# Kernel optimization log

Hardware: AMD Instinct MI355X
Metric: run time of the kernel (lower is better)

The kernel has to match this reference:

```python
import jax, jax.numpy as jnp
import numpy as np

A = 100000   # batched action space size
V = 500000   # relation vocab
D = 128      # ExperimentSettings.dim
L = 64       # question token count


def setup_inputs() -> dict:
    key = jax.random.key(0)
    ks = jax.random.split(key, 8)
    return {
        "action_ids": jax.random.randint(ks[0], (A,), 0, V),
        "emb_table": jax.random.normal(ks[1], (V, D), dtype=jnp.float32) * 0.1,
        "question_t": jax.random.normal(ks[2], (L, D), dtype=jnp.float32),
        "history_t": jax.random.normal(ks[3], (D,), dtype=jnp.float32),
        "W1": jax.random.normal(ks[4], (D, 2 * D), dtype=jnp.float32) * 0.05,
        "b1": jnp.zeros((D,), dtype=jnp.float32),
        "W2": jax.random.normal(ks[5], (D, D), dtype=jnp.float32) * 0.05,
        "b2": jnp.zeros((D,), dtype=jnp.float32),
    }


def reference(action_ids, emb_table, question_t, history_t, W1, b1, W2, b2):
    # per-action relation embedding lookup (batched over the action space)
    rel = emb_table[action_ids]                              # [A, D]
    # attention over question tokens, keyed by the relation embedding
    att = jnp.einsum("ld,ad->al", question_t, rel)           # [A, L]
    w = jax.nn.softmax(att, axis=-1)
    question = jnp.einsum("al,ld->ad", w, question_t)        # [A, D]
    # Perceptron(dim, dim, 2*dim): MLP on [history; question], dotted with rel
    hist = jnp.broadcast_to(history_t, question.shape)       # [A, D]
    x = jnp.concatenate([hist, question], axis=-1)           # [A, 2D]
    hidden = jax.nn.relu(x @ W1.T + b1)                      # [A, D]
    out = hidden @ W2.T + b2                                 # [A, D]
    scores = jnp.sum(rel * out, axis=-1)                     # [A]
    return jax.nn.softmax(scores, axis=0)
```

## Files before the change

kernel.cpp:

```cpp
#include <hip/hip_runtime.h>
#include <math.h>


#define BA   64
#define NTHR 256

typedef float          f32x4  __attribute__((ext_vector_type(4)));
typedef short          bf16x8 __attribute__((ext_vector_type(8)));
typedef unsigned short us4v   __attribute__((ext_vector_type(4)));

#define RELo 0
#define R1o  8704
#define R2o  17408
#define R3o  26624
#define NB   31232

__device__ __forceinline__ unsigned short f2bf(float f) {
    unsigned int u = __float_as_uint(f);
    return (unsigned short)((u + 0x7fffu + ((u >> 16) & 1u)) >> 16);
}
__device__ __forceinline__ float bf2f(unsigned short h) {
    return __uint_as_float(((unsigned int)h) << 16);
}

__global__ void k_prep(const float* __restrict__ hist, const float* __restrict__ W1,
                       const float* __restrict__ b1, float* __restrict__ h1)
{
    const int lane = threadIdx.x & 63;
    const int w    = threadIdx.x >> 6;
    const float h0  = hist[lane];
    const float h64 = hist[64 + lane];
    #pragma unroll 4
    for (int r = 0; r < 32; ++r) {
        const int j = w * 32 + r;
        float p = fmaf(W1[j * 256 + lane], h0, W1[j * 256 + 64 + lane] * h64);
        #pragma unroll
        for (int o = 1; o < 64; o <<= 1) p += __shfl_xor(p, o);
        if (lane == 0) h1[j] = b1[j] + p;
    }
}

__global__ void __launch_bounds__(NTHR, 2)
k_main(const int* __restrict__ action_ids,
       const float* __restrict__ emb,
       const float* __restrict__ Qg,
       const float* __restrict__ W1,
       const float* __restrict__ W2,
       const float* __restrict__ b2,
       const float* __restrict__ h1g,
       float* __restrict__ scores,
       float* __restrict__ mb,
       float* __restrict__ sb,
       int A)
{
    __shared__ __align__(16) unsigned short B_[NB];
    __shared__ float h1s[128];
    __shared__ float b2s[128];
    __shared__ float stash[BA];

    const int tid  = threadIdx.x;
    const int a0   = blockIdx.x * BA;
    const int w    = tid >> 6;
    const int lane = tid & 63;
    const int c    = lane & 15;
    const int g    = lane >> 4;

    {
        const int l = tid >> 2, seg = tid & 3;
        const float4* qs = (const float4*)&Qg[l * 128 + seg * 32];
        unsigned short qb[32];
        #pragma unroll
        for (int j = 0; j < 8; ++j) {
            const float4 v = qs[j];
            qb[j*4+0] = f2bf(v.x); qb[j*4+1] = f2bf(v.y);
            qb[j*4+2] = f2bf(v.z); qb[j*4+3] = f2bf(v.w);
            us4v p = { qb[j*4+0], qb[j*4+1], qb[j*4+2], qb[j*4+3] };
            *(us4v*)&B_[R1o + l * 136 + seg * 32 + j * 4] = p;
        }
        #pragma unroll
        for (int i = 0; i < 32; ++i)
            B_[R2o + (seg * 32 + i) * 72 + l] = qb[i];

        const int ga  = a0 + l;
        const int rid = (ga < A) ? action_ids[ga] : 0;
        const float4* es = (const float4*)&emb[(size_t)rid * 128 + seg * 32];
        #pragma unroll
        for (int j = 0; j < 8; ++j) {
            const float4 v = es[j];
            us4v p = { f2bf(v.x), f2bf(v.y), f2bf(v.z), f2bf(v.w) };
            *(us4v*)&B_[RELo + l * 136 + seg * 32 + j * 4] = p;
        }
        if (tid < 128) h1s[tid] = h1g[tid];
        else           b2s[tid - 128] = b2[tid - 128];
    }
    __syncthreads();

    f32x4 att[4] = {};
    #pragma unroll
    for (int ks = 0; ks < 4; ++ks) {
        const bf16x8 afr = *(const bf16x8*)&B_[RELo + (16*w + c)*136 + ks*32 + g*8];
        #pragma unroll
        for (int nt = 0; nt < 4; ++nt) {
            const bf16x8 bfr = *(const bf16x8*)&B_[R1o + (16*nt + c)*136 + ks*32 + g*8];
            att[nt] = __builtin_amdgcn_mfma_f32_16x16x32_bf16(afr, bfr, att[nt], 0, 0, 0);
        }
    }

    {
        float m[4] = { -INFINITY, -INFINITY, -INFINITY, -INFINITY };
        #pragma unroll
        for (int nt = 0; nt < 4; ++nt)
            #pragma unroll
            for (int r = 0; r < 4; ++r) m[r] = fmaxf(m[r], att[nt][r]);
        #pragma unroll
        for (int r = 0; r < 4; ++r) {
            m[r] = fmaxf(m[r], __shfl_xor(m[r], 1));
            m[r] = fmaxf(m[r], __shfl_xor(m[r], 2));
            m[r] = fmaxf(m[r], __shfl_xor(m[r], 4));
            m[r] = fmaxf(m[r], __shfl_xor(m[r], 8));
        }
        float s[4] = { 0.f, 0.f, 0.f, 0.f };
        #pragma unroll
        for (int nt = 0; nt < 4; ++nt)
            #pragma unroll
            for (int r = 0; r < 4; ++r) {
                att[nt][r] = __expf(att[nt][r] - m[r]);
                s[r] += att[nt][r];
            }
        #pragma unroll
        for (int r = 0; r < 4; ++r) {
            s[r] += __shfl_xor(s[r], 1);
            s[r] += __shfl_xor(s[r], 2);
            s[r] += __shfl_xor(s[r], 4);
            s[r] += __shfl_xor(s[r], 8);
            s[r] = 1.f / s[r];
        }
        #pragma unroll
        for (int nt = 0; nt < 4; ++nt)
            #pragma unroll
            for (int r = 0; r < 4; ++r)
                B_[R3o + (16*w + 4*g + r)*72 + 16*nt + c] =
                    f2bf(att[nt][r] * s[r]);
    }

    f32x4 qacc[8] = {};
    #pragma unroll
    for (int ks = 0; ks < 2; ++ks) {
        const bf16x8 afr = *(const bf16x8*)&B_[R3o + (16*w + c)*72 + ks*32 + g*8];
        #pragma unroll
        for (int nt = 0; nt < 8; ++nt) {
            const bf16x8 bfr = *(const bf16x8*)&B_[R2o + (16*nt + c)*72 + ks*32 + g*8];
            qacc[nt] = __builtin_amdgcn_mfma_f32_16x16x32_bf16(afr, bfr, qacc[nt], 0, 0, 0);
        }
    }
    __syncthreads();

    #pragma unroll
    for (int nt = 0; nt < 8; ++nt)
        #pragma unroll
        for (int r = 0; r < 4; ++r)
            B_[R1o + (16*w + 4*g + r)*136 + 16*nt + c] = f2bf(qacc[nt][r]);

    f32x4 hacc[8] = {};
    for (int ch = 0; ch < 4; ++ch) {
        if (ch) __syncthreads();
        {
            const int jl = tid >> 3, seg = tid & 7;
            const float4* src = (const float4*)&W1[(ch*32 + jl)*256 + 128 + seg*16];
            #pragma unroll
            for (int j = 0; j < 4; ++j) {
                const float4 v = src[j];
                us4v p = { f2bf(v.x), f2bf(v.y), f2bf(v.z), f2bf(v.w) };
                *(us4v*)&B_[R3o + jl*136 + seg*16 + j*4] = p;
            }
        }
        __syncthreads();
        #pragma unroll
        for (int ks = 0; ks < 4; ++ks) {
            const bf16x8 afr = *(const bf16x8*)&B_[R1o + (16*w + c)*136 + ks*32 + g*8];
            #pragma unroll
            for (int nt = 0; nt < 2; ++nt) {
                const bf16x8 bfr = *(const bf16x8*)&B_[R3o + (16*nt + c)*136 + ks*32 + g*8];
                hacc[ch*2+nt] = __builtin_amdgcn_mfma_f32_16x16x32_bf16(afr, bfr, hacc[ch*2+nt], 0, 0, 0);
            }
        }
    }
    __syncthreads();

    #pragma unroll
    for (int ch = 0; ch < 4; ++ch)
        #pragma unroll
        for (int nt = 0; nt < 2; ++nt) {
            const int j = ch*32 + nt*16 + c;
            const float hb = h1s[j];
            #pragma unroll
            for (int r = 0; r < 4; ++r) {
                const float hv = fmaxf(hacc[ch*2+nt][r] + hb, 0.f);
                B_[R2o + (16*w + 4*g + r)*136 + j] = f2bf(hv);
            }
        }

    float sacc[4] = { 0.f, 0.f, 0.f, 0.f };
    for (int ch = 0; ch < 4; ++ch) {
        if (ch) __syncthreads();
        {
            const int dl = tid >> 3, seg = tid & 7;
            const float4* src = (const float4*)&W2[(ch*32 + dl)*128 + seg*16];
            #pragma unroll
            for (int j = 0; j < 4; ++j) {
                const float4 v = src[j];
                us4v p = { f2bf(v.x), f2bf(v.y), f2bf(v.z), f2bf(v.w) };
                *(us4v*)&B_[R3o + dl*136 + seg*16 + j*4] = p;
            }
        }
        __syncthreads();
        f32x4 oacc[2] = {};
        #pragma unroll
        for (int ks = 0; ks < 4; ++ks) {
            const bf16x8 afr = *(const bf16x8*)&B_[R2o + (16*w + c)*136 + ks*32 + g*8];
            #pragma unroll
            for (int nt = 0; nt < 2; ++nt) {
                const bf16x8 bfr = *(const bf16x8*)&B_[R3o + (16*nt + c)*136 + ks*32 + g*8];
                oacc[nt] = __builtin_amdgcn_mfma_f32_16x16x32_bf16(afr, bfr, oacc[nt], 0, 0, 0);
            }
        }
        #pragma unroll
        for (int nt = 0; nt < 2; ++nt) {
            const int d = ch*32 + nt*16 + c;
            const float bb = b2s[d];
            #pragma unroll
            for (int r = 0; r < 4; ++r) {
                const float ov = oacc[nt][r] + bb;
                const float rv = bf2f(B_[RELo + (16*w + 4*g + r)*136 + d]);
                sacc[r] = fmaf(ov, rv, sacc[r]);
            }
        }
    }

    #pragma unroll
    for (int r = 0; r < 4; ++r) {
        sacc[r] += __shfl_xor(sacc[r], 1);
        sacc[r] += __shfl_xor(sacc[r], 2);
        sacc[r] += __shfl_xor(sacc[r], 4);
        sacc[r] += __shfl_xor(sacc[r], 8);
    }
    if (c == 0) {
        #pragma unroll
        for (int r = 0; r < 4; ++r) {
            const int al = 16*w + 4*g + r;
            const int ga = a0 + al;
            if (ga < A) scores[ga] = sacc[r];
            stash[al] = sacc[r];
        }
    }
    __syncthreads();

    if (tid < 64) {
        const bool valid = (a0 + tid) < A;
        float sv = valid ? stash[tid] : -INFINITY;
        float m = sv;
        #pragma unroll
        for (int o = 1; o < 64; o <<= 1) m = fmaxf(m, __shfl_xor(m, o));
        float ex = valid ? __expf(sv - m) : 0.f;
        #pragma unroll
        for (int o = 1; o < 64; o <<= 1) ex += __shfl_xor(ex, o);
        if (tid == 0) { mb[blockIdx.x] = m; sb[blockIdx.x] = ex; }
    }
}

__global__ void k_combine(const float* __restrict__ mb, const float* __restrict__ sb,
                          int n, float* __restrict__ MS)
{
    __shared__ float red[256];
    const int tid = threadIdx.x;
    float m = -INFINITY;
    for (int i = tid; i < n; i += 256) m = fmaxf(m, mb[i]);
    red[tid] = m; __syncthreads();
    for (int s = 128; s > 0; s >>= 1) {
        if (tid < s) red[tid] = fmaxf(red[tid], red[tid + s]);
        __syncthreads();
    }
    const float M = red[0];
    __syncthreads();
    float sum = 0.f;
    for (int i = tid; i < n; i += 256) sum += sb[i] * __expf(mb[i] - M);
    red[tid] = sum; __syncthreads();
    for (int s = 128; s > 0; s >>= 1) {
        if (tid < s) red[tid] += red[tid + s];
        __syncthreads();
    }
    if (tid == 0) { MS[0] = M; MS[1] = 1.f / red[0]; }
}

__global__ void k_norm(const float* __restrict__ scores, const float* __restrict__ MS,
                       float* __restrict__ out, int A)
{
    const int i = blockIdx.x * blockDim.x + threadIdx.x;
    if (i < A) out[i] = __expf(scores[i] - MS[0]) * MS[1];
}

extern "C" void kernel_launch(void* const* d_in, const int* in_sizes, int n_in,
                              void* d_out, int out_size, void* d_ws, size_t ws_size,
                              hipStream_t stream)
{
    const int*   action_ids = (const int*)  d_in[0];
    const float* emb        = (const float*)d_in[1];
    const float* Qg         = (const float*)d_in[2];
    const float* hist       = (const float*)d_in[3];
    const float* W1         = (const float*)d_in[4];
    const float* b1         = (const float*)d_in[5];
    const float* W2         = (const float*)d_in[6];
    const float* b2         = (const float*)d_in[7];
    float* out = (float*)d_out;
    const int A    = in_sizes[0];
    const int nblk = (A + BA - 1) / BA;

    float* ws  = (float*)d_ws;
    float* h1  = ws;
    float* MS  = ws + 128;
    const int nal = (nblk + 255) & ~255;
    float* mbp = ws + 256;
    float* sbp = mbp + nal;
    (void)n_in; (void)out_size; (void)ws_size;

    k_prep<<<1, 256, 0, stream>>>(hist, W1, b1, h1);
    k_main<<<nblk, NTHR, 0, stream>>>(action_ids, emb, Qg, W1, W2, b2, h1,
                                      out, mbp, sbp, A);
    k_combine<<<1, 256, 0, stream>>>(mbp, sbp, nblk, MS);
    k_norm<<<(A + 255) / 256, 256, 0, stream>>>(out, MS, out, A);
}
```

Measured before the change: 388.9 us.

## Preconvert weights to bf16 once and make each wave independent without block syncs

A new pre-kernel converts Q, Q transpose, and the W1/W2 halves to bf16 in workspace once per call. The main kernel then reads MFMA B-fragments directly from global/L2 instead of staging and converting weights in LDS every block. Each wave now owns its own 16-row LDS slice, which removes all __syncthreads. LDS use drops enough to raise the launch-bounds occupancy to 4, and softmax partials are emitted per wave. The cost is an extra launch and more scattered global fragment loads that depend on L2 caching.

```diff
diff --git a/kernel.cpp b/kernel.cpp
--- a/kernel.cpp
+++ b/kernel.cpp
@@ -4,22 +4,18 @@
 
 #define BA   64
 #define NTHR 256
-
-typedef float          f32x4  __attribute__((ext_vector_type(4)));
-typedef short          bf16x8 __attribute__((ext_vector_type(8)));
-typedef unsigned short us4v   __attribute__((ext_vector_type(4)));
-
-#define RELo 0
-#define R1o  8704
-#define R2o  17408
-#define R3o  26624
-#define NB   31232
-
-__device__ __forceinline__ unsigned short f2bf(float f) {
+typedef unsigned short ushort_t;
+typedef float  f32x4  __attribute__((ext_vector_type(4)));
+typedef short  bf16x8 __attribute__((ext_vector_type(8)));
+
+#define WSTRIDE 4352
+#define LDS_USH (4 * WSTRIDE)
+
+__device__ __forceinline__ ushort_t f2bf(float f) {
     unsigned int u = __float_as_uint(f);
-    return (unsigned short)((u + 0x7fffu + ((u >> 16) & 1u)) >> 16);
-}
-__device__ __forceinline__ float bf2f(unsigned short h) {
+    return (ushort_t)((u + 0x7fffu + ((u >> 16) & 1u)) >> 16);
+}
+__device__ __forceinline__ float bf2f(ushort_t h) {
     return __uint_as_float(((unsigned int)h) << 16);
 }
 
@@ -40,71 +36,78 @@
     }
 }
 
-__global__ void __launch_bounds__(NTHR, 2)
+__global__ void k_cvt(const float* __restrict__ Qg, const float* __restrict__ W1,
+                      const float* __restrict__ W2,
+                      ushort_t* __restrict__ Qbf, ushort_t* __restrict__ QTbf,
+                      ushort_t* __restrict__ W1bf, ushort_t* __restrict__ W2bf)
+{
+    const int i = blockIdx.x * 256 + threadIdx.x;
+    if (i < 16384) {
+        W1bf[i] = f2bf(W1[(i >> 7) * 256 + 128 + (i & 127)]);
+    } else if (i < 32768) {
+        const int k = i - 16384;
+        W2bf[k] = f2bf(W2[k]);
+    } else if (i < 40960) {
+        const int k = i - 32768;
+        Qbf[k] = f2bf(Qg[k]);
+    } else {
+        const int k = i - 40960;
+        const int d = k >> 6, l = k & 63;
+        QTbf[k] = f2bf(Qg[l * 128 + d]);
+    }
+}
+
+__global__ void __launch_bounds__(NTHR, 4)
 k_main(const int* __restrict__ action_ids,
        const float* __restrict__ emb,
-       const float* __restrict__ Qg,
-       const float* __restrict__ W1,
-       const float* __restrict__ W2,
        const float* __restrict__ b2,
        const float* __restrict__ h1g,
+       const ushort_t* __restrict__ Qbf,
+       const ushort_t* __restrict__ QTbf,
+       const ushort_t* __restrict__ W1bf,
+       const ushort_t* __restrict__ W2bf,
        float* __restrict__ scores,
        float* __restrict__ mb,
        float* __restrict__ sb,
        int A)
 {
-    __shared__ __align__(16) unsigned short B_[NB];
-    __shared__ float h1s[128];
-    __shared__ float b2s[128];
-    __shared__ float stash[BA];
-
+    __shared__ __align__(16) ushort_t L[LDS_USH];
     const int tid  = threadIdx.x;
-    const int a0   = blockIdx.x * BA;
     const int w    = tid >> 6;
     const int lane = tid & 63;
     const int c    = lane & 15;
     const int g    = lane >> 4;
-
+    ushort_t* RELw = &L[w * WSTRIDE];
+    ushort_t* SCRw = &L[w * WSTRIDE + 2176];
+    const int a0   = blockIdx.x * BA + 16 * w;
+
+    bf16x8 relA[4];
     {
-        const int l = tid >> 2, seg = tid & 3;
-        const float4* qs = (const float4*)&Qg[l * 128 + seg * 32];
-        unsigned short qb[32];
-        #pragma unroll
-        for (int j = 0; j < 8; ++j) {
-            const float4 v = qs[j];
-            qb[j*4+0] = f2bf(v.x); qb[j*4+1] = f2bf(v.y);
-            qb[j*4+2] = f2bf(v.z); qb[j*4+3] = f2bf(v.w);
-            us4v p = { qb[j*4+0], qb[j*4+1], qb[j*4+2], qb[j*4+3] };
-            *(us4v*)&B_[R1o + l * 136 + seg * 32 + j * 4] = p;
-        }
-        #pragma unroll
-        for (int i = 0; i < 32; ++i)
-            B_[R2o + (seg * 32 + i) * 72 + l] = qb[i];
-
-        const int ga  = a0 + l;
+        const int ga  = a0 + c;
         const int rid = (ga < A) ? action_ids[ga] : 0;
-        const float4* es = (const float4*)&emb[(size_t)rid * 128 + seg * 32];
-        #pragma unroll
-        for (int j = 0; j < 8; ++j) {
-            const float4 v = es[j];
-            us4v p = { f2bf(v.x), f2bf(v.y), f2bf(v.z), f2bf(v.w) };
-            *(us4v*)&B_[RELo + l * 136 + seg * 32 + j * 4] = p;
-        }
-        if (tid < 128) h1s[tid] = h1g[tid];
-        else           b2s[tid - 128] = b2[tid - 128];
-    }
-    __syncthreads();
+        const float* er = emb + (size_t)rid * 128;
+        #pragma unroll
+        for (int ks = 0; ks < 4; ++ks) {
+            const float4 v0 = *(const float4*)&er[ks * 32 + g * 8];
+            const float4 v1 = *(const float4*)&er[ks * 32 + g * 8 + 4];
+            union { bf16x8 v; ushort_t u[8]; } p;
+            p.u[0] = f2bf(v0.x); p.u[1] = f2bf(v0.y);
+            p.u[2] = f2bf(v0.z); p.u[3] = f2bf(v0.w);
+            p.u[4] = f2bf(v1.x); p.u[5] = f2bf(v1.y);
+            p.u[6] = f2bf(v1.z); p.u[7] = f2bf(v1.w);
+            relA[ks] = p.v;
+            *(bf16x8*)&RELw[c * 136 + ks * 32 + g * 8] = p.v;
+        }
+    }
 
     f32x4 att[4] = {};
     #pragma unroll
-    for (int ks = 0; ks < 4; ++ks) {
-        const bf16x8 afr = *(const bf16x8*)&B_[RELo + (16*w + c)*136 + ks*32 + g*8];
+    for (int ks = 0; ks < 4; ++ks)
         #pragma unroll
         for (int nt = 0; nt < 4; ++nt) {
-            const bf16x8 bfr = *(const bf16x8*)&B_[R1o + (16*nt + c)*136 + ks*32 + g*8];
-            att[nt] = __builtin_amdgcn_mfma_f32_16x16x32_bf16(afr, bfr, att[nt], 0, 0, 0);
-        }
-    }
+            const bf16x8 bfr = *(const bf16x8*)&Qbf[(16*nt + c) * 128 + ks*32 + g*8];
+            att[nt] = __builtin_amdgcn_mfma_f32_16x16x32_bf16(relA[ks], bfr, att[nt], 0, 0, 0);
+        }
 
     {
         float m[4] = { -INFINITY, -INFINITY, -INFINITY, -INFINITY };
@@ -139,104 +142,64 @@
         for (int nt = 0; nt < 4; ++nt)
             #pragma unroll
             for (int r = 0; r < 4; ++r)
-                B_[R3o + (16*w + 4*g + r)*72 + 16*nt + c] =
-                    f2bf(att[nt][r] * s[r]);
+                SCRw[(4*g + r) * 72 + 16*nt + c] = f2bf(att[nt][r] * s[r]);
     }
 
     f32x4 qacc[8] = {};
     #pragma unroll
     for (int ks = 0; ks < 2; ++ks) {
-        const bf16x8 afr = *(const bf16x8*)&B_[R3o + (16*w + c)*72 + ks*32 + g*8];
+        const bf16x8 afr = *(const bf16x8*)&SCRw[c * 72 + ks*32 + g*8];
         #pragma unroll
         for (int nt = 0; nt < 8; ++nt) {
-            const bf16x8 bfr = *(const bf16x8*)&B_[R2o + (16*nt + c)*72 + ks*32 + g*8];
+            const bf16x8 bfr = *(const bf16x8*)&QTbf[(16*nt + c) * 64 + ks*32 + g*8];
             qacc[nt] = __builtin_amdgcn_mfma_f32_16x16x32_bf16(afr, bfr, qacc[nt], 0, 0, 0);
         }
     }
-    __syncthreads();
-
     #pragma unroll
     for (int nt = 0; nt < 8; ++nt)
         #pragma unroll
         for (int r = 0; r < 4; ++r)
-            B_[R1o + (16*w + 4*g + r)*136 + 16*nt + c] = f2bf(qacc[nt][r]);
+            SCRw[(4*g + r) * 136 + 16*nt + c] = f2bf(qacc[nt][r]);
 
     f32x4 hacc[8] = {};
-    for (int ch = 0; ch < 4; ++ch) {
-        if (ch) __syncthreads();
-        {
-            const int jl = tid >> 3, seg = tid & 7;
-            const float4* src = (const float4*)&W1[(ch*32 + jl)*256 + 128 + seg*16];
-            #pragma unroll
-            for (int j = 0; j < 4; ++j) {
-                const float4 v = src[j];
-                us4v p = { f2bf(v.x), f2bf(v.y), f2bf(v.z), f2bf(v.w) };
-                *(us4v*)&B_[R3o + jl*136 + seg*16 + j*4] = p;
-            }
-        }
-        __syncthreads();
-        #pragma unroll
-        for (int ks = 0; ks < 4; ++ks) {
-            const bf16x8 afr = *(const bf16x8*)&B_[R1o + (16*w + c)*136 + ks*32 + g*8];
-            #pragma unroll
-            for (int nt = 0; nt < 2; ++nt) {
-                const bf16x8 bfr = *(const bf16x8*)&B_[R3o + (16*nt + c)*136 + ks*32 + g*8];
-                hacc[ch*2+nt] = __builtin_amdgcn_mfma_f32_16x16x32_bf16(afr, bfr, hacc[ch*2+nt], 0, 0, 0);
-            }
-        }
-    }
-    __syncthreads();
-
-    #pragma unroll
-    for (int ch = 0; ch < 4; ++ch)
-        #pragma unroll
-        for (int nt = 0; nt < 2; ++nt) {
-            const int j = ch*32 + nt*16 + c;
-            const float hb = h1s[j];
-            #pragma unroll
-            for (int r = 0; r < 4; ++r) {
-                const float hv = fmaxf(hacc[ch*2+nt][r] + hb, 0.f);
-                B_[R2o + (16*w + 4*g + r)*136 + j] = f2bf(hv);
-            }
-        }
-
+    #pragma unroll
+    for (int ks = 0; ks < 4; ++ks) {
+        const bf16x8 afr = *(const bf16x8*)&SCRw[c * 136 + ks*32 + g*8];
+        #pragma unroll
+        for (int nt = 0; nt < 8; ++nt) {
+            const bf16x8 bfr = *(const bf16x8*)&W1bf[(16*nt + c) * 128 + ks*32 + g*8];
+            hacc[nt] = __builtin_amdgcn_mfma_f32_16x16x32_bf16(afr, bfr, hacc[nt], 0, 0, 0);
+        }
+    }
+    #pragma unroll
+    for (int nt = 0; nt < 8; ++nt) {
+        const float hb = h1g[16*nt + c];
+        #pragma unroll
+        for (int r = 0; r < 4; ++r)
+            SCRw[(4*g + r) * 136 + 16*nt + c] = f2bf(fmaxf(hacc[nt][r] + hb, 0.f));
+    }
+
+    f32x4 oacc[8] = {};
+    #pragma unroll
+    for (int ks = 0; ks < 4; ++ks) {
+        const bf16x8 afr = *(const bf16x8*)&SCRw[c * 136 + ks*32 + g*8];
+        #pragma unroll
+        for (int nt = 0; nt < 8; ++nt) {
+            const bf16x8 bfr = *(const bf16x8*)&W2bf[(16*nt + c) * 128 + ks*32 + g*8];
+            oacc[nt] = __builtin_amdgcn_mfma_f32_16x16x32_bf16(afr, bfr, oacc[nt], 0, 0, 0);
+        }
+    }
     float sacc[4] = { 0.f, 0.f, 0.f, 0.f };
-    for (int ch = 0; ch < 4; ++ch) {
-        if (ch) __syncthreads();
-        {
-            const int dl = tid >> 3, seg = tid & 7;
-            const float4* src = (const float4*)&W2[(ch*32 + dl)*128 + seg*16];
-            #pragma unroll
-            for (int j = 0; j < 4; ++j) {
-                const float4 v = src[j];
-                us4v p = { f2bf(v.x), f2bf(v.y), f2bf(v.z), f2bf(v.w) };
-                *(us4v*)&B_[R3o + dl*136 + seg*16 + j*4] = p;
-            }
-        }
-        __syncthreads();
-        f32x4 oacc[2] = {};
-        #pragma unroll
-        for (int ks = 0; ks < 4; ++ks) {
-            const bf16x8 afr = *(const bf16x8*)&B_[R2o + (16*w + c)*136 + ks*32 + g*8];
-            #pragma unroll
-            for (int nt = 0; nt < 2; ++nt) {
-                const bf16x8 bfr = *(const bf16x8*)&B_[R3o + (16*nt + c)*136 + ks*32 + g*8];
-                oacc[nt] = __builtin_amdgcn_mfma_f32_16x16x32_bf16(afr, bfr, oacc[nt], 0, 0, 0);
-            }
-        }
-        #pragma unroll
-        for (int nt = 0; nt < 2; ++nt) {
-            const int d = ch*32 + nt*16 + c;
-            const float bb = b2s[d];
-            #pragma unroll
-            for (int r = 0; r < 4; ++r) {
-                const float ov = oacc[nt][r] + bb;
-                const float rv = bf2f(B_[RELo + (16*w + 4*g + r)*136 + d]);
-                sacc[r] = fmaf(ov, rv, sacc[r]);
-            }
-        }
-    }
-
+    #pragma unroll
+    for (int nt = 0; nt < 8; ++nt) {
+        const float bb = b2[16*nt + c];
+        #pragma unroll
+        for (int r = 0; r < 4; ++r) {
+            const float ov = oacc[nt][r] + bb;
+            const float rv = bf2f(RELw[(4*g + r) * 136 + 16*nt + c]);
+            sacc[r] = fmaf(ov, rv, sacc[r]);
+        }
+    }
     #pragma unroll
     for (int r = 0; r < 4; ++r) {
         sacc[r] += __shfl_xor(sacc[r], 1);
@@ -247,24 +210,29 @@
     if (c == 0) {
         #pragma unroll
         for (int r = 0; r < 4; ++r) {
-            const int al = 16*w + 4*g + r;
-            const int ga = a0 + al;
+            const int ga = a0 + 4*g + r;
             if (ga < A) scores[ga] = sacc[r];
-            stash[al] = sacc[r];
-        }
-    }
-    __syncthreads();
-
-    if (tid < 64) {
-        const bool valid = (a0 + tid) < A;
-        float sv = valid ? stash[tid] : -INFINITY;
-        float m = sv;
-        #pragma unroll
-        for (int o = 1; o < 64; o <<= 1) m = fmaxf(m, __shfl_xor(m, o));
-        float ex = valid ? __expf(sv - m) : 0.f;
-        #pragma unroll
-        for (int o = 1; o < 64; o <<= 1) ex += __shfl_xor(ex, o);
-        if (tid == 0) { mb[blockIdx.x] = m; sb[blockIdx.x] = ex; }
+        }
+    }
+
+    {
+        float m = -INFINITY;
+        #pragma unroll
+        for (int r = 0; r < 4; ++r)
+            if (a0 + 4*g + r < A) m = fmaxf(m, sacc[r]);
+        m = fmaxf(m, __shfl_xor(m, 16));
+        m = fmaxf(m, __shfl_xor(m, 32));
+        float es = 0.f;
+        #pragma unroll
+        for (int r = 0; r < 4; ++r)
+            if (a0 + 4*g + r < A) es += __expf(sacc[r] - m);
+        es += __shfl_xor(es, 16);
+        es += __shfl_xor(es, 32);
+        if (lane == 0) {
+            const int idx = blockIdx.x * 4 + w;
+            mb[idx] = m;
+            sb[idx] = es;
+        }
     }
 }
 
@@ -314,18 +282,26 @@
     float* out = (float*)d_out;
     const int A    = in_sizes[0];
     const int nblk = (A + BA - 1) / BA;
+    const int npar = nblk * 4;
 
     float* ws  = (float*)d_ws;
     float* h1  = ws;
     float* MS  = ws + 128;
-    const int nal = (nblk + 255) & ~255;
+    const int nal = (npar + 255) & ~255;
     float* mbp = ws + 256;
     float* sbp = mbp + nal;
+    ushort_t* u0   = (ushort_t*)(sbp + nal);
+    ushort_t* Qbf  = u0;
+    ushort_t* QTbf = u0 + 8192;
+    ushort_t* W1bf = u0 + 16384;
+    ushort_t* W2bf = u0 + 32768;
     (void)n_in; (void)out_size; (void)ws_size;
 
     k_prep<<<1, 256, 0, stream>>>(hist, W1, b1, h1);
-    k_main<<<nblk, NTHR, 0, stream>>>(action_ids, emb, Qg, W1, W2, b2, h1,
+    k_cvt <<<192, 256, 0, stream>>>(Qg, W1, W2, Qbf, QTbf, W1bf, W2bf);
+    k_main<<<nblk, NTHR, 0, stream>>>(action_ids, emb, b2, h1,
+                                      Qbf, QTbf, W1bf, W2bf,
                                       out, mbp, sbp, A);
-    k_combine<<<1, 256, 0, stream>>>(mbp, sbp, nblk, MS);
+    k_combine<<<1, 256, 0, stream>>>(mbp, sbp, npar, MS);
     k_norm<<<(A + 255) / 256, 256, 0, stream>>>(out, MS, out, A);
 }
```

Measured after the change: 442.2 us. 13.7% more time.
